# Optimization experiments

Hardware: AMD Instinct MI355X
Metric: run time of the kernel (lower is better)

The kernel has to match this reference:

```python
import jax, jax.numpy as jnp
import numpy as np
import math

D_MODEL = 1024
NUM_HEADS = 16
D_K = D_MODEL // NUM_HEADS
MAX_SEQ_LEN = 2048
THETA = 10000.0
BATCH = 2
SEQ = 2048


def setup_inputs() -> dict:
    key = jax.random.key(0)
    ks = jax.random.split(key, 5)
    std = math.sqrt(2.0 / (D_MODEL + D_MODEL))
    def w(k):
        return jnp.clip(std * jax.random.normal(k, (D_MODEL, D_MODEL), dtype=jnp.float32), -3 * std, 3 * std)
    return {
        "x": jax.random.normal(ks[0], (BATCH, SEQ, D_MODEL), dtype=jnp.float32),
        "token_positions": jnp.arange(SEQ, dtype=jnp.int32),
        "Wq": w(ks[1]),
        "Wk": w(ks[2]),
        "Wv": w(ks[3]),
        "Wo": w(ks[4]),
    }


def _rope_tables():
    inv_freq = 1.0 / THETA ** (jnp.arange(0, D_K, 2, dtype=jnp.float32) / D_K)  # [d_k/2]
    positions = jnp.arange(MAX_SEQ_LEN, dtype=jnp.float32)[:, None]             # [max_seq, 1]
    angles = positions * inv_freq                                               # [max_seq, d_k/2]
    return jnp.cos(angles), jnp.sin(angles)


def _apply_rope(x, cos, sin):
    # x: [..., seq, d_k]; cos/sin: [seq, d_k/2] (broadcast over leading dims)
    x1, x2 = x[..., ::2], x[..., 1::2]
    r1 = x1 * cos - x2 * sin
    r2 = x1 * sin + x2 * cos
    return jnp.stack((r1, r2), axis=-1).reshape(x.shape)


def reference(x, token_positions, Wq, Wk, Wv, Wo):
    B, S, D = x.shape
    def proj(W):
        y = jnp.einsum('bsd,od->bso', x, W)
        return y.reshape(B, S, NUM_HEADS, D_K).transpose(0, 2, 1, 3)  # [B,H,S,dk]
    q, k, v = proj(Wq), proj(Wk), proj(Wv)

    cos_t, sin_t = _rope_tables()
    cos, sin = cos_t[token_positions], sin_t[token_positions]  # [S, d_k/2]
    q = _apply_rope(q, cos, sin)
    k = _apply_rope(k, cos, sin)

    scores = jnp.einsum('bhqd,bhkd->bhqk', q, k) / math.sqrt(D_K)
    causal = jnp.tril(jnp.ones((S, S), dtype=bool))
    scores = jnp.where(causal, scores, -jnp.inf)
    attn = jax.nn.softmax(scores, axis=-1)
    out = jnp.einsum('bhqk,bhkd->bhqd', attn, v)
    out = out.transpose(0, 2, 1, 3).reshape(B, S, D)
    return jnp.einsum('bsd,od->bso', out, Wo)
```

## Files before the change

kernel.cpp:

```cpp
#include <hip/hip_runtime.h>
#include <hip/hip_bf16.h>


typedef __attribute__((ext_vector_type(8))) short short8;
typedef __attribute__((ext_vector_type(4))) float floatx4;

static __device__ __forceinline__ unsigned short f2bf(float f) {
  __hip_bfloat16 h = __float2bfloat16(f);
  return *(unsigned short*)&h;
}

static __device__ __forceinline__ unsigned int pk2bf(float a, float b) {
  unsigned int ua = __float_as_uint(a) + 0x8000u;
  unsigned int ub = __float_as_uint(b) + 0x8000u;
  return __builtin_amdgcn_perm(ub, ua, 0x07060302u);
}

static __device__ __forceinline__ float fexp2(float x) {
  float r;
  asm("v_exp_f32 %0, %1\n\ts_nop 0" : "=v"(r) : "v"(x));
  return r;
}

static __device__ __forceinline__ void gl2lds16(const unsigned short* g,
                                                unsigned short* l) {
  __builtin_amdgcn_global_load_lds(
      (const __attribute__((address_space(1))) void*)g,
      (__attribute__((address_space(3))) void*)l, 16, 0, 0);
}

__global__ __launch_bounds__(256) void cvt_all(
    const float4* __restrict__ x,  const float4* __restrict__ wq,
    const float4* __restrict__ wk, const float4* __restrict__ wv,
    const float4* __restrict__ wo,
    ushort4* __restrict__ xb,  ushort4* __restrict__ wqb,
    ushort4* __restrict__ wkb, ushort4* __restrict__ wvb,
    ushort4* __restrict__ wob,
    const int* __restrict__ tokpos,
    float* __restrict__ ctab, float* __restrict__ stab) {
  int t = blockIdx.y;
  int i = blockIdx.x * 256 + threadIdx.x;
  if (t == 5) {
    if (i < 65536) {
      int s = i >> 5, f = i & 31;
      float inv = expf(-9.210340371976184f * (float)(2 * f) / 64.0f);
      float ang = (float)tokpos[s] * inv;
      ctab[i] = cosf(ang);
      stab[i] = sinf(ang);
    }
    return;
  }
  const float4* s = (t == 0) ? x : (t == 1) ? wq : (t == 2) ? wk : (t == 3) ? wv : wo;
  ushort4* d = (t == 0) ? xb : (t == 1) ? wqb : (t == 2) ? wkb : (t == 3) ? wvb : wob;
  int n4 = (t == 0) ? 1048576 : 262144;
  if (i < n4) {
    float4 v = s[i];
    ushort4 o;
    o.x = f2bf(v.x); o.y = f2bf(v.y); o.z = f2bf(v.z); o.w = f2bf(v.w);
    d[i] = o;
  }
}

__global__ __launch_bounds__(256) void qkv_mfma(
    const unsigned short* __restrict__ X,
    const unsigned short* __restrict__ Wq,
    const unsigned short* __restrict__ Wk,
    const unsigned short* __restrict__ Wv,
    const float* __restrict__ ctab, const float* __restrict__ stab,
    unsigned short* __restrict__ Qo, unsigned short* __restrict__ Ko,
    unsigned short* __restrict__ Vo) {
  int mat = blockIdx.z;
  const unsigned short* W = (mat == 0) ? Wq : ((mat == 1) ? Wk : Wv);
  unsigned short* Out = (mat == 0) ? Qo : ((mat == 1) ? Ko : Vo);
  int m0 = blockIdx.x * 64, n0 = blockIdx.y * 128;

  __shared__ __align__(16) unsigned short lA[2][64 * 64];
  __shared__ __align__(16) unsigned short lB[2][128 * 64];
  int tid = threadIdx.x;
  int wave = tid >> 6, lane = tid & 63;
  int l15 = lane & 15, quad = lane >> 4;
  int rsub = lane >> 3, sch = lane & 7;
  int fsw = l15 & 7;

  floatx4 acc[4][2];
#pragma unroll
  for (int m = 0; m < 4; ++m)
#pragma unroll
    for (int n = 0; n < 2; ++n) acc[m][n] = (floatx4){0.f, 0.f, 0.f, 0.f};

#pragma unroll
  for (int kp = 0; kp < 2; ++kp) {
#pragma unroll
    for (int p = 0; p < 2; ++p) {
      int r = wave * 16 + p * 8 + rsub;
      int g = sch ^ (r & 7);
      gl2lds16(X + (size_t)(m0 + r) * 1024 + kp * 64 + g * 8,
               lA[kp] + (wave * 16 + p * 8) * 64);
    }
#pragma unroll
    for (int p = 0; p < 4; ++p) {
      int r = wave * 32 + p * 8 + rsub;
      int g = sch ^ (r & 7);
      gl2lds16(W + (size_t)(n0 + r) * 1024 + kp * 64 + g * 8,
               lB[kp] + (wave * 32 + p * 8) * 64);
    }
  }
  asm volatile("s_waitcnt vmcnt(6)" ::: "memory");
  __builtin_amdgcn_s_barrier();

  for (int kt = 0; kt < 16; ++kt) {
    int cur = kt & 1;
#pragma unroll
    for (int ks = 0; ks < 2; ++ks) {
      int slot = ((ks * 4 + quad) ^ fsw) * 8;
      short8 af[4], bf[2];
#pragma unroll
      for (int m = 0; m < 4; ++m)
        af[m] = *(const short8*)(lA[cur] + (m * 16 + l15) * 64 + slot);
#pragma unroll
      for (int n = 0; n < 2; ++n)
        bf[n] = *(const short8*)(lB[cur] + (wave * 32 + n * 16 + l15) * 64 + slot);
#pragma unroll
      for (int m = 0; m < 4; ++m)
#pragma unroll
        for (int n = 0; n < 2; ++n)
          acc[m][n] = __builtin_amdgcn_mfma_f32_16x16x32_bf16(
              af[m], bf[n], acc[m][n], 0, 0, 0);
    }
    if (kt == 15) break;
    __builtin_amdgcn_s_barrier();
    if (kt < 14) {
#pragma unroll
      for (int p = 0; p < 2; ++p) {
        int r = wave * 16 + p * 8 + rsub;
        int g = sch ^ (r & 7);
        gl2lds16(X + (size_t)(m0 + r) * 1024 + (kt + 2) * 64 + g * 8,
                 lA[cur] + (wave * 16 + p * 8) * 64);
      }
#pragma unroll
      for (int p = 0; p < 4; ++p) {
        int r = wave * 32 + p * 8 + rsub;
        int g = sch ^ (r & 7);
        gl2lds16(W + (size_t)(n0 + r) * 1024 + (kt + 2) * 64 + g * 8,
                 lB[cur] + (wave * 32 + p * 8) * 64);
      }
      asm volatile("s_waitcnt vmcnt(6)" ::: "memory");
    } else {
      asm volatile("s_waitcnt vmcnt(0)" ::: "memory");
    }
    __builtin_amdgcn_s_barrier();
  }

#pragma unroll
  for (int n = 0; n < 2; ++n) {
    int col = n0 + wave * 32 + n * 16 + l15;
    int h = col >> 6;
    int d = col & 63;
    int pi = d >> 1;
    bool odd = (d & 1) != 0;
    size_t hb = (size_t)h * 2048 * 64;
#pragma unroll
    for (int m = 0; m < 4; ++m) {
      int row0 = m0 + m * 16 + quad * 4;
      int b = row0 >> 11;
      int s0 = row0 & 2047;
      size_t base = (size_t)b * 16 * 2048 * 64 + hb;
      if (mat == 2) {
        ushort4 pv;
        pv.x = f2bf(acc[m][n][0]);
        pv.y = f2bf(acc[m][n][1]);
        pv.z = f2bf(acc[m][n][2]);
        pv.w = f2bf(acc[m][n][3]);
        *(ushort4*)(Out + base + (size_t)d * 2048 + s0) = pv;
      } else {
#pragma unroll
        for (int i = 0; i < 4; ++i) {
          int s = s0 + i;
          float v = acc[m][n][i];
          float p = __shfl_xor(v, 1);
          float c = ctab[s * 32 + pi];
          float sn = stab[s * 32 + pi];
          float res = odd ? fmaf(p, sn, v * c) : fmaf(v, c, -p * sn);
          if (mat == 0) res *= 0.1803368801111204f;
          Out[base + (size_t)s * 64 + d] = f2bf(res);
        }
      }
    }
  }
}

__global__ __launch_bounds__(256) void oproj_mfma(
    const unsigned short* __restrict__ A, const unsigned short* __restrict__ Wo,
    float* __restrict__ Out) {
  __shared__ __align__(16) unsigned short lA[2][64 * 64];
  __shared__ __align__(16) unsigned short lB[2][128 * 64];
  int tid = threadIdx.x;
  int wave = tid >> 6, lane = tid & 63;
  int l15 = lane & 15, quad = lane >> 4;
  int rsub = lane >> 3, sch = lane & 7;
  int fsw = l15 & 7;
  int m0 = blockIdx.x * 64, n0 = blockIdx.y * 128;

  floatx4 acc[4][2];
#pragma unroll
  for (int m = 0; m < 4; ++m)
#pragma unroll
    for (int n = 0; n < 2; ++n) acc[m][n] = (floatx4){0.f, 0.f, 0.f, 0.f};

#pragma unroll
  for (int kp = 0; kp < 2; ++kp) {
#pragma unroll
    for (int p = 0; p < 2; ++p) {
      int r = wave * 16 + p * 8 + rsub;
      int g = sch ^ (r & 7);
      gl2lds16(A + (size_t)(m0 + r) * 1024 + kp * 64 + g * 8,
               lA[kp] + (wave * 16 + p * 8) * 64);
    }
#pragma unroll
    for (int p = 0; p < 4; ++p) {
      int r = wave * 32 + p * 8 + rsub;
      int g = sch ^ (r & 7);
      gl2lds16(Wo + (size_t)(n0 + r) * 1024 + kp * 64 + g * 8,
               lB[kp] + (wave * 32 + p * 8) * 64);
    }
  }
  asm volatile("s_waitcnt vmcnt(6)" ::: "memory");
  __builtin_amdgcn_s_barrier();

  for (int kt = 0; kt < 16; ++kt) {
    int cur = kt & 1;
#pragma unroll
    for (int ks = 0; ks < 2; ++ks) {
      int slot = ((ks * 4 + quad) ^ fsw) * 8;
      short8 af[4], bf[2];
#pragma unroll
      for (int m = 0; m < 4; ++m)
        af[m] = *(const short8*)(lA[cur] + (m * 16 + l15) * 64 + slot);
#pragma unroll
      for (int n = 0; n < 2; ++n)
        bf[n] = *(const short8*)(lB[cur] + (wave * 32 + n * 16 + l15) * 64 + slot);
#pragma unroll
      for (int m = 0; m < 4; ++m)
#pragma unroll
        for (int n = 0; n < 2; ++n)
          acc[m][n] = __builtin_amdgcn_mfma_f32_16x16x32_bf16(
              af[m], bf[n], acc[m][n], 0, 0, 0);
    }
    if (kt == 15) break;
    __builtin_amdgcn_s_barrier();
    if (kt < 14) {
#pragma unroll
      for (int p = 0; p < 2; ++p) {
        int r = wave * 16 + p * 8 + rsub;
        int g = sch ^ (r & 7);
        gl2lds16(A + (size_t)(m0 + r) * 1024 + (kt + 2) * 64 + g * 8,
                 lA[cur] + (wave * 16 + p * 8) * 64);
      }
#pragma unroll
      for (int p = 0; p < 4; ++p) {
        int r = wave * 32 + p * 8 + rsub;
        int g = sch ^ (r & 7);
        gl2lds16(Wo + (size_t)(n0 + r) * 1024 + (kt + 2) * 64 + g * 8,
                 lB[cur] + (wave * 32 + p * 8) * 64);
      }
      asm volatile("s_waitcnt vmcnt(6)" ::: "memory");
    } else {
      asm volatile("s_waitcnt vmcnt(0)" ::: "memory");
    }
    __builtin_amdgcn_s_barrier();
  }

#pragma unroll
  for (int m = 0; m < 4; ++m) {
#pragma unroll
    for (int n = 0; n < 2; ++n) {
      int col = n0 + wave * 32 + n * 16 + l15;
#pragma unroll
      for (int i = 0; i < 4; ++i) {
        int row = m0 + m * 16 + quad * 4 + i;
        Out[(size_t)row * 1024 + col] = acc[m][n][i];
      }
    }
  }
}

#define LPS 72

static __device__ __forceinline__ void qk_step(
    const unsigned short* lK, int l15, int c0, int c1,
    short8 q0, short8 q1, floatx4 (&sc)[4]) {
#pragma unroll
  for (int sub = 0; sub < 4; ++sub) {
    const unsigned short* kr = lK + (sub * 16 + l15) * 64;
    short8 a0 = *(const short8*)(kr + c0);
    short8 a1 = *(const short8*)(kr + c1);
    floatx4 s = {0.f, 0.f, 0.f, 0.f};
    s = __builtin_amdgcn_mfma_f32_16x16x32_bf16(a0, q0, s, 0, 0, 0);
    s = __builtin_amdgcn_mfma_f32_16x16x32_bf16(a1, q1, s, 0, 0, 0);
    sc[sub] = s;
  }
}

static __device__ __forceinline__ void sm_step(
    floatx4 (&sc)[4], float& m_i, float& l_i, floatx4 (&o)[4],
    bool diag, int qin, int quad) {
  if (diag) {
#pragma unroll
    for (int sub = 0; sub < 4; ++sub)
#pragma unroll
      for (int i = 0; i < 4; ++i)
        if (sub * 16 + quad * 4 + i > qin) sc[sub][i] = -1e30f;
  }
  float mb = sc[0][0];
#pragma unroll
  for (int sub = 0; sub < 4; ++sub)
#pragma unroll
    for (int i = 0; i < 4; ++i) mb = fmaxf(mb, sc[sub][i]);
  mb = fmaxf(mb, __shfl_xor(mb, 16));
  mb = fmaxf(mb, __shfl_xor(mb, 32));

  float mn = fmaxf(m_i, mb);
  float al = fexp2(m_i - mn);
  m_i = mn;
  float rs = 0.f;
#pragma unroll
  for (int sub = 0; sub < 4; ++sub)
#pragma unroll
    for (int i = 0; i < 4; ++i) {
      float p = fexp2(sc[sub][i] - mn);
      sc[sub][i] = p;
      rs += p;
    }
  rs += __shfl_xor(rs, 16);
  rs += __shfl_xor(rs, 32);
  l_i = l_i * al + rs;
#pragma unroll
  for (int n = 0; n < 4; ++n) {
    o[n][0] *= al; o[n][1] *= al; o[n][2] *= al; o[n][3] *= al;
  }
}

static __device__ __forceinline__ void pv_step(
    const floatx4 (&sc)[4], floatx4 (&o)[4], unsigned short* lPw,
    const unsigned short* lV, int l15, int quad, int c0, int c1) {
  unsigned short* pw = lPw + l15 * LPS;
#pragma unroll
  for (int sub = 0; sub < 4; ++sub) {
    uint2 w;
    w.x = pk2bf(sc[sub][0], sc[sub][1]);
    w.y = pk2bf(sc[sub][2], sc[sub][3]);
    *(uint2*)(pw + sub * 16 + quad * 4) = w;
  }
  const unsigned short* pr = lPw + l15 * LPS + quad * 8;
  short8 pa0 = *(const short8*)(pr);
  short8 pa1 = *(const short8*)(pr + 32);
#pragma unroll
  for (int n = 0; n < 4; ++n) {
    const unsigned short* vr = lV + (n * 16 + l15) * 64;
    short8 vb0 = *(const short8*)(vr + c0);
    short8 vb1 = *(const short8*)(vr + c1);
    o[n] = __builtin_amdgcn_mfma_f32_16x16x32_bf16(vb0, pa0, o[n], 0, 0, 0);
    o[n] = __builtin_amdgcn_mfma_f32_16x16x32_bf16(vb1, pa1, o[n], 0, 0, 0);
  }
}

__global__ __launch_bounds__(256, 2) void attn_flash(
    const unsigned short* __restrict__ Q, const unsigned short* __restrict__ K,
    const unsigned short* __restrict__ Vt, unsigned short* __restrict__ Oc) {
  __shared__ __align__(16) unsigned short lK[64 * 64];
  __shared__ __align__(16) unsigned short lV[64 * 64];
  __shared__ unsigned short lP[8][16 * LPS];

  int tid = threadIdx.x;
  int wave = tid >> 6, lane = tid & 63;
  int l15 = lane & 15, quad = lane >> 4;

  int id = blockIdx.x;
  int rest = id >> 3;
  int pair = rest >> 2;
  int bh = (id & 7) * 4 + (rest & 3);
  int tA = pair;
  int tB = 31 - pair;
  int NT = tB + 1;

  size_t base = (size_t)bh * 2048 * 64;

  const unsigned short* qrowA = Q + base + (size_t)(tA * 64 + wave * 16 + l15) * 64;
  const unsigned short* qrowB = Q + base + (size_t)(tB * 64 + wave * 16 + l15) * 64;
  short8 qA0 = *(const short8*)(qrowA + quad * 8);
  short8 qA1 = *(const short8*)(qrowA + 32 + quad * 8);
  short8 qB0 = *(const short8*)(qrowB + quad * 8);
  short8 qB1 = *(const short8*)(qrowB + 32 + quad * 8);

  floatx4 oA[4], oB[4];
  float mA_i = -1e30f, lA_i = 0.f, mB_i = -1e30f, lB_i = 0.f;
#pragma unroll
  for (int n = 0; n < 4; ++n) {
    oA[n] = (floatx4){0.f, 0.f, 0.f, 0.f};
    oB[n] = (floatx4){0.f, 0.f, 0.f, 0.f};
  }

  int r0 = tid >> 3, g = tid & 7;
  int r1 = r0 + 32;
  int e0 = g * 8;
  int sl = (g ^ (r0 & 7)) * 8;
  int fsw = l15 & 7;
  int c0 = (quad ^ fsw) * 8;
  int c1 = ((quad + 4) ^ fsw) * 8;

  const unsigned short* kp = K + base;
  const unsigned short* vp = Vt + base;
  short8 pk0 = *(const short8*)(kp + r0 * 64 + e0);
  short8 pk1 = *(const short8*)(kp + r1 * 64 + e0);
  short8 pv0 = *(const short8*)(vp + (size_t)r0 * 2048 + e0);
  short8 pv1 = *(const short8*)(vp + (size_t)r1 * 2048 + e0);

  int qin = wave * 16 + l15;

  for (int kt = 0; kt < NT; ++kt) {
    bool aAct = (kt <= tA);

    __syncthreads();
    *(short8*)(lK + r0 * 64 + sl) = pk0;
    *(short8*)(lK + r1 * 64 + sl) = pk1;
    *(short8*)(lV + r0 * 64 + sl) = pv0;
    *(short8*)(lV + r1 * 64 + sl) = pv1;
    __syncthreads();

    if (kt + 1 < NT) {
      const unsigned short* kn = K + base + (size_t)(kt + 1) * 4096;
      const unsigned short* vn = Vt + base + (kt + 1) * 64;
      pk0 = *(const short8*)(kn + r0 * 64 + e0);
      pk1 = *(const short8*)(kn + r1 * 64 + e0);
      pv0 = *(const short8*)(vn + (size_t)r0 * 2048 + e0);
      pv1 = *(const short8*)(vn + (size_t)r1 * 2048 + e0);
    }

    floatx4 scB[4], scA[4];
    qk_step(lK, l15, c0, c1, qB0, qB1, scB);
    if (aAct) qk_step(lK, l15, c0, c1, qA0, qA1, scA);

    sm_step(scB, mB_i, lB_i, oB, kt == NT - 1, qin, quad);
    if (aAct) sm_step(scA, mA_i, lA_i, oA, kt == tA, qin, quad);

    pv_step(scB, oB, lP[wave * 2], lV, l15, quad, c0, c1);
    if (aAct) pv_step(scA, oA, lP[wave * 2 + 1], lV, l15, quad, c0, c1);
  }

  int b = bh >> 4, h = bh & 15;
  {
    float inv = 1.f / lB_i;
    int s = tB * 64 + wave * 16 + l15;
    size_t orow = (size_t)(b * 2048 + s) * 1024 + h * 64;
#pragma unroll
    for (int n = 0; n < 4; ++n) {
      uint2 ov;
      ov.x = pk2bf(oB[n][0] * inv, oB[n][1] * inv);
      ov.y = pk2bf(oB[n][2] * inv, oB[n][3] * inv);
      *(uint2*)(Oc + orow + n * 16 + quad * 4) = ov;
    }
  }
  {
    float inv = 1.f / lA_i;
    int s = tA * 64 + wave * 16 + l15;
    size_t orow = (size_t)(b * 2048 + s) * 1024 + h * 64;
#pragma unroll
    for (int n = 0; n < 4; ++n) {
      uint2 ov;
      ov.x = pk2bf(oA[n][0] * inv, oA[n][1] * inv);
      ov.y = pk2bf(oA[n][2] * inv, oA[n][3] * inv);
      *(uint2*)(Oc + orow + n * 16 + quad * 4) = ov;
    }
  }
}

extern "C" void kernel_launch(void* const* d_in, const int* in_sizes, int n_in,
                              void* d_out, int out_size, void* d_ws, size_t ws_size,
                              hipStream_t stream) {
  const float* x  = (const float*)d_in[0];
  const int* tokpos = (const int*)d_in[1];
  const float* Wq = (const float*)d_in[2];
  const float* Wk = (const float*)d_in[3];
  const float* Wv = (const float*)d_in[4];
  const float* Wo = (const float*)d_in[5];
  float* out = (float*)d_out;

  float* ws = (float*)d_ws;
  float* ctab = ws;
  float* stab = ctab + 65536;
  unsigned short* u = (unsigned short*)(stab + 65536);
  unsigned short* Qb  = u;
  unsigned short* Kb  = Qb + 4194304;
  unsigned short* Vb  = Kb + 4194304;
  unsigned short* Oc  = Vb + 4194304;
  unsigned short* xb  = Oc + 4194304;
  unsigned short* Wqb = xb + 4194304;
  unsigned short* Wkb = Wqb + 1048576;
  unsigned short* Wvb = Wkb + 1048576;
  unsigned short* Wob = Wvb + 1048576;

  cvt_all<<<dim3(4096, 6), 256, 0, stream>>>(
      (const float4*)x, (const float4*)Wq, (const float4*)Wk,
      (const float4*)Wv, (const float4*)Wo,
      (ushort4*)xb, (ushort4*)Wqb, (ushort4*)Wkb, (ushort4*)Wvb, (ushort4*)Wob,
      tokpos, ctab, stab);

  qkv_mfma<<<dim3(64, 8, 3), 256, 0, stream>>>(
      xb, Wqb, Wkb, Wvb, ctab, stab, Qb, Kb, Vb);
  attn_flash<<<dim3(512), 256, 0, stream>>>(Qb, Kb, Vb, Oc);
  oproj_mfma<<<dim3(64, 8), 256, 0, stream>>>(Oc, Wob, out);
}
```

Measured before the change: 174.6 us.

## Double-buffer K/V in LDS, halve attention block size, swizzle P buffer

```diff
diff --git a/kernel.cpp b/kernel.cpp
--- a/kernel.cpp
+++ b/kernel.cpp
@@ -284,8 +284,6 @@
   }
 }
 
-#define LPS 72
-
 static __device__ __forceinline__ void qk_step(
     const unsigned short* lK, int l15, int c0, int c1,
     short8 q0, short8 q1, floatx4 (&sc)[4]) {
@@ -341,19 +339,20 @@
 }
 
 static __device__ __forceinline__ void pv_step(
-    const floatx4 (&sc)[4], floatx4 (&o)[4], unsigned short* lPw,
+    const floatx4 (&sc)[4], floatx4 (&o)[4], unsigned short* lPws,
     const unsigned short* lV, int l15, int quad, int c0, int c1) {
-  unsigned short* pw = lPw + l15 * LPS;
+  int swz = l15 & 7;
+  unsigned short* pw = lPws + l15 * 64;
 #pragma unroll
   for (int sub = 0; sub < 4; ++sub) {
     uint2 w;
     w.x = pk2bf(sc[sub][0], sc[sub][1]);
     w.y = pk2bf(sc[sub][2], sc[sub][3]);
-    *(uint2*)(pw + sub * 16 + quad * 4) = w;
-  }
-  const unsigned short* pr = lPw + l15 * LPS + quad * 8;
-  short8 pa0 = *(const short8*)(pr);
-  short8 pa1 = *(const short8*)(pr + 32);
+    int slot = (sub * 2 + (quad >> 1)) ^ swz;
+    *(uint2*)(pw + slot * 8 + (quad & 1) * 4) = w;
+  }
+  short8 pa0 = *(const short8*)(pw + ((quad ^ swz) * 8));
+  short8 pa1 = *(const short8*)(pw + (((4 + quad) ^ swz) * 8));
 #pragma unroll
   for (int n = 0; n < 4; ++n) {
     const unsigned short* vr = lV + (n * 16 + l15) * 64;
@@ -364,29 +363,30 @@
   }
 }
 
-__global__ __launch_bounds__(256, 2) void attn_flash(
+__global__ __launch_bounds__(128, 2) void attn_flash(
     const unsigned short* __restrict__ Q, const unsigned short* __restrict__ K,
     const unsigned short* __restrict__ Vt, unsigned short* __restrict__ Oc) {
-  __shared__ __align__(16) unsigned short lK[64 * 64];
-  __shared__ __align__(16) unsigned short lV[64 * 64];
-  __shared__ unsigned short lP[8][16 * LPS];
+  __shared__ __align__(16) unsigned short lK[2][64 * 64];
+  __shared__ __align__(16) unsigned short lV[2][64 * 64];
+  __shared__ __align__(16) unsigned short lP[4][16 * 64];
 
   int tid = threadIdx.x;
   int wave = tid >> 6, lane = tid & 63;
   int l15 = lane & 15, quad = lane >> 4;
 
   int id = blockIdx.x;
-  int rest = id >> 3;
-  int pair = rest >> 2;
-  int bh = (id & 7) * 4 + (rest & 3);
-  int tA = pair;
-  int tB = 31 - pair;
+  int bh = (id & 7) * 4 + ((id >> 3) & 3);
+  int rem = id >> 5;
+  int pair = rem >> 1;
+  int h = rem & 1;
+  int tA = pair, tB = 31 - pair;
   int NT = tB + 1;
 
   size_t base = (size_t)bh * 2048 * 64;
-
-  const unsigned short* qrowA = Q + base + (size_t)(tA * 64 + wave * 16 + l15) * 64;
-  const unsigned short* qrowB = Q + base + (size_t)(tB * 64 + wave * 16 + l15) * 64;
+  int qoff = h * 32 + wave * 16 + l15;
+
+  const unsigned short* qrowA = Q + base + (size_t)(tA * 64 + qoff) * 64;
+  const unsigned short* qrowB = Q + base + (size_t)(tB * 64 + qoff) * 64;
   short8 qA0 = *(const short8*)(qrowA + quad * 8);
   short8 qA1 = *(const short8*)(qrowA + 32 + quad * 8);
   short8 qB0 = *(const short8*)(qrowB + quad * 8);
@@ -401,57 +401,102 @@
   }
 
   int r0 = tid >> 3, g = tid & 7;
-  int r1 = r0 + 32;
   int e0 = g * 8;
   int sl = (g ^ (r0 & 7)) * 8;
   int fsw = l15 & 7;
   int c0 = (quad ^ fsw) * 8;
   int c1 = ((quad + 4) ^ fsw) * 8;
 
-  const unsigned short* kp = K + base;
-  const unsigned short* vp = Vt + base;
-  short8 pk0 = *(const short8*)(kp + r0 * 64 + e0);
-  short8 pk1 = *(const short8*)(kp + r1 * 64 + e0);
-  short8 pv0 = *(const short8*)(vp + (size_t)r0 * 2048 + e0);
-  short8 pv1 = *(const short8*)(vp + (size_t)r1 * 2048 + e0);
-
-  int qin = wave * 16 + l15;
+  short8 pk0, pk1, pk2, pk3, pv0, pv1, pv2, pv3;
+
+  {
+    const unsigned short* kp = K + base;
+    const unsigned short* vp = Vt + base;
+    pk0 = *(const short8*)(kp + (r0 +  0) * 64 + e0);
+    pk1 = *(const short8*)(kp + (r0 + 16) * 64 + e0);
+    pk2 = *(const short8*)(kp + (r0 + 32) * 64 + e0);
+    pk3 = *(const short8*)(kp + (r0 + 48) * 64 + e0);
+    pv0 = *(const short8*)(vp + (size_t)(r0 +  0) * 2048 + e0);
+    pv1 = *(const short8*)(vp + (size_t)(r0 + 16) * 2048 + e0);
+    pv2 = *(const short8*)(vp + (size_t)(r0 + 32) * 2048 + e0);
+    pv3 = *(const short8*)(vp + (size_t)(r0 + 48) * 2048 + e0);
+  }
+  *(short8*)(lK[0] + (r0 +  0) * 64 + sl) = pk0;
+  *(short8*)(lK[0] + (r0 + 16) * 64 + sl) = pk1;
+  *(short8*)(lK[0] + (r0 + 32) * 64 + sl) = pk2;
+  *(short8*)(lK[0] + (r0 + 48) * 64 + sl) = pk3;
+  *(short8*)(lV[0] + (r0 +  0) * 64 + sl) = pv0;
+  *(short8*)(lV[0] + (r0 + 16) * 64 + sl) = pv1;
+  *(short8*)(lV[0] + (r0 + 32) * 64 + sl) = pv2;
+  *(short8*)(lV[0] + (r0 + 48) * 64 + sl) = pv3;
+  {
+    const unsigned short* kp = K + base + 4096;
+    const unsigned short* vp = Vt + base + 64;
+    pk0 = *(const short8*)(kp + (r0 +  0) * 64 + e0);
+    pk1 = *(const short8*)(kp + (r0 + 16) * 64 + e0);
+    pk2 = *(const short8*)(kp + (r0 + 32) * 64 + e0);
+    pk3 = *(const short8*)(kp + (r0 + 48) * 64 + e0);
+    pv0 = *(const short8*)(vp + (size_t)(r0 +  0) * 2048 + e0);
+    pv1 = *(const short8*)(vp + (size_t)(r0 + 16) * 2048 + e0);
+    pv2 = *(const short8*)(vp + (size_t)(r0 + 32) * 2048 + e0);
+    pv3 = *(const short8*)(vp + (size_t)(r0 + 48) * 2048 + e0);
+  }
+  asm volatile("s_waitcnt lgkmcnt(0)" ::: "memory");
+  __builtin_amdgcn_s_barrier();
+  __builtin_amdgcn_sched_barrier(0);
+
+  int qin = qoff;
 
   for (int kt = 0; kt < NT; ++kt) {
+    int cur = kt & 1;
     bool aAct = (kt <= tA);
-
-    __syncthreads();
-    *(short8*)(lK + r0 * 64 + sl) = pk0;
-    *(short8*)(lK + r1 * 64 + sl) = pk1;
-    *(short8*)(lV + r0 * 64 + sl) = pv0;
-    *(short8*)(lV + r1 * 64 + sl) = pv1;
-    __syncthreads();
-
-    if (kt + 1 < NT) {
-      const unsigned short* kn = K + base + (size_t)(kt + 1) * 4096;
-      const unsigned short* vn = Vt + base + (kt + 1) * 64;
-      pk0 = *(const short8*)(kn + r0 * 64 + e0);
-      pk1 = *(const short8*)(kn + r1 * 64 + e0);
-      pv0 = *(const short8*)(vn + (size_t)r0 * 2048 + e0);
-      pv1 = *(const short8*)(vn + (size_t)r1 * 2048 + e0);
-    }
+    const unsigned short* lKc = lK[cur];
+    const unsigned short* lVc = lV[cur];
 
     floatx4 scB[4], scA[4];
-    qk_step(lK, l15, c0, c1, qB0, qB1, scB);
-    if (aAct) qk_step(lK, l15, c0, c1, qA0, qA1, scA);
+    qk_step(lKc, l15, c0, c1, qB0, qB1, scB);
+    if (aAct) qk_step(lKc, l15, c0, c1, qA0, qA1, scA);
 
     sm_step(scB, mB_i, lB_i, oB, kt == NT - 1, qin, quad);
     if (aAct) sm_step(scA, mA_i, lA_i, oA, kt == tA, qin, quad);
 
-    pv_step(scB, oB, lP[wave * 2], lV, l15, quad, c0, c1);
-    if (aAct) pv_step(scA, oA, lP[wave * 2 + 1], lV, l15, quad, c0, c1);
-  }
-
-  int b = bh >> 4, h = bh & 15;
+    pv_step(scB, oB, lP[wave * 2], lVc, l15, quad, c0, c1);
+    if (aAct) pv_step(scA, oA, lP[wave * 2 + 1], lVc, l15, quad, c0, c1);
+
+    if (kt + 1 < NT) {
+      unsigned short* wK = lK[cur ^ 1];
+      unsigned short* wV = lV[cur ^ 1];
+      *(short8*)(wK + (r0 +  0) * 64 + sl) = pk0;
+      *(short8*)(wK + (r0 + 16) * 64 + sl) = pk1;
+      *(short8*)(wK + (r0 + 32) * 64 + sl) = pk2;
+      *(short8*)(wK + (r0 + 48) * 64 + sl) = pk3;
+      *(short8*)(wV + (r0 +  0) * 64 + sl) = pv0;
+      *(short8*)(wV + (r0 + 16) * 64 + sl) = pv1;
+      *(short8*)(wV + (r0 + 32) * 64 + sl) = pv2;
+      *(short8*)(wV + (r0 + 48) * 64 + sl) = pv3;
+      if (kt + 2 < NT) {
+        const unsigned short* kp = K + base + (size_t)(kt + 2) * 4096;
+        const unsigned short* vp = Vt + base + (size_t)(kt + 2) * 64;
+        pk0 = *(const short8*)(kp + (r0 +  0) * 64 + e0);
+        pk1 = *(const short8*)(kp + (r0 + 16) * 64 + e0);
+        pk2 = *(const short8*)(kp + (r0 + 32) * 64 + e0);
+        pk3 = *(const short8*)(kp + (r0 + 48) * 64 + e0);
+        pv0 = *(const short8*)(vp + (size_t)(r0 +  0) * 2048 + e0);
+        pv1 = *(const short8*)(vp + (size_t)(r0 + 16) * 2048 + e0);
+        pv2 = *(const short8*)(vp + (size_t)(r0 + 32) * 2048 + e0);
+        pv3 = *(const short8*)(vp + (size_t)(r0 + 48) * 2048 + e0);
+      }
+      asm volatile("s_waitcnt lgkmcnt(0)" ::: "memory");
+      __builtin_amdgcn_s_barrier();
+      __builtin_amdgcn_sched_barrier(0);
+    }
+  }
+
+  int b = bh >> 4, hh = bh & 15;
   {
     float inv = 1.f / lB_i;
-    int s = tB * 64 + wave * 16 + l15;
-    size_t orow = (size_t)(b * 2048 + s) * 1024 + h * 64;
+    int s = tB * 64 + qoff;
+    size_t orow = (size_t)(b * 2048 + s) * 1024 + hh * 64;
 #pragma unroll
     for (int n = 0; n < 4; ++n) {
       uint2 ov;
@@ -462,8 +507,8 @@
   }
   {
     float inv = 1.f / lA_i;
-    int s = tA * 64 + wave * 16 + l15;
-    size_t orow = (size_t)(b * 2048 + s) * 1024 + h * 64;
+    int s = tA * 64 + qoff;
+    size_t orow = (size_t)(b * 2048 + s) * 1024 + hh * 64;
 #pragma unroll
     for (int n = 0; n < 4; ++n) {
       uint2 ov;
@@ -507,6 +552,6 @@
 
   qkv_mfma<<<dim3(64, 8, 3), 256, 0, stream>>>(
       xb, Wqb, Wkb, Wvb, ctab, stab, Qb, Kb, Vb);
-  attn_flash<<<dim3(512), 256, 0, stream>>>(Qb, Kb, Vb, Oc);
+  attn_flash<<<dim3(1024), 128, 0, stream>>>(Qb, Kb, Vb, Oc);
   oproj_mfma<<<dim3(64, 8), 256, 0, stream>>>(Oc, Wob, out);
 }
```

New measurement: 174.0 us. Within noise of the previous version (-0.3%).
